# Optimization experiments

Measured on AMD Instinct MI355X. Metric: run time of the kernel, lower is better.

## Reference

```python
import jax, jax.numpy as jnp
import numpy as np

N = 50000
NEG_SLOPE = 0.2


def add_self_loops(edge_index, n):
    loops = jnp.arange(n, dtype=edge_index.dtype)
    return jnp.concatenate([edge_index, jnp.stack([loops, loops])], axis=1)


def gat_layer(x, edge_index, W, a_src, a_dst, b, heads, ch):
    # x: [N, F_in], W: [F_in, heads*ch], a_src/a_dst: [heads, ch], b: [heads*ch]
    n = x.shape[0]
    src, dst = edge_index[0], edge_index[1]
    h = (x @ W).reshape(n, heads, ch)                      # [N, H, C]
    alpha_src = jnp.sum(h * a_src, axis=-1)                # [N, H]
    alpha_dst = jnp.sum(h * a_dst, axis=-1)                # [N, H]
    e = jax.nn.leaky_relu(alpha_src[src] + alpha_dst[dst], NEG_SLOPE)  # [E, H]
    # segment softmax over incoming edges of each destination node
    m = jax.ops.segment_max(e, dst, num_segments=n)        # [N, H]
    ex = jnp.exp(e - m[dst])                               # [E, H]
    denom = jax.ops.segment_sum(ex, dst, num_segments=n)   # [N, H]
    alpha = ex / (denom[dst] + 1e-16)                      # [E, H]
    msg = h[src] * alpha[:, :, None]                       # [E, H, C]
    out = jax.ops.segment_sum(msg, dst, num_segments=n)    # [N, H, C]
    return out.reshape(n, heads * ch) + b


def setup_inputs() -> dict:
    key = jax.random.key(0)
    ks = jax.random.split(key, 12)
    input_dim, hidden_dim, output_dim, heads = 128, 32, 64, 4
    E = 1600000
    x = jax.random.normal(ks[0], (N, input_dim), dtype=jnp.float32)
    edge_index = jax.random.randint(ks[1], (2, E), 0, N, dtype=jnp.int64)
    s1 = 1.0 / np.sqrt(input_dim)
    s2 = 1.0 / np.sqrt(hidden_dim * heads)
    W1 = jax.random.uniform(ks[2], (input_dim, heads * hidden_dim), jnp.float32, -s1, s1)
    a_src1 = jax.random.uniform(ks[3], (heads, hidden_dim), jnp.float32, -s1, s1)
    a_dst1 = jax.random.uniform(ks[4], (heads, hidden_dim), jnp.float32, -s1, s1)
    b1 = jnp.zeros((heads * hidden_dim,), jnp.float32)
    W2 = jax.random.uniform(ks[5], (heads * hidden_dim, output_dim), jnp.float32, -s2, s2)
    a_src2 = jax.random.uniform(ks[6], (1, output_dim), jnp.float32, -s2, s2)
    a_dst2 = jax.random.uniform(ks[7], (1, output_dim), jnp.float32, -s2, s2)
    b2 = jnp.zeros((output_dim,), jnp.float32)
    return {"x": x, "edge_index": edge_index,
            "W1": W1, "a_src1": a_src1, "a_dst1": a_dst1, "b1": b1,
            "W2": W2, "a_src2": a_src2, "a_dst2": a_dst2, "b2": b2}


def reference(x, edge_index, W1, a_src1, a_dst1, b1, W2, a_src2, a_dst2, b2):
    n = x.shape[0]
    ei = add_self_loops(edge_index, n)
    h = gat_layer(x, ei, W1, a_src1, a_dst1, b1, heads=4, ch=32)
    h = jax.nn.relu(h)
    out = gat_layer(h, ei, W2, a_src2, a_dst2, b2, heads=1, ch=64)
    return out
```

## Files before the change

### kernel.cpp

```cpp
#include <hip/hip_runtime.h>
#include <hip/hip_bf16.h>
#include <hip/hip_fp16.h>


#define LRELU_SLOPE 0.2f
#define NBMAX 200
#define NBLK  512
#define BCAP  16384
#define CAPIMG 16384

typedef _Float16 f16x8 __attribute__((ext_vector_type(8)));
typedef _Float16 f16x4 __attribute__((ext_vector_type(4)));
typedef float f32x4 __attribute__((ext_vector_type(4)));


__global__ __launch_bounds__(256) void hist_kernel(const int* __restrict__ ei_dst,
                                                   int* __restrict__ hist, int E, int chunk) {
    __shared__ int h[NBMAX];
    int t = threadIdx.x;
    for (int i = t; i < NBMAX; i += 256) h[i] = 0;
    __syncthreads();
    int begin = blockIdx.x * chunk;
    int endE = min(E, begin + chunk);
    for (int e = begin + t; e < endE; e += 256) atomicAdd(&h[ei_dst[e] >> 8], 1);
    __syncthreads();
    for (int i = t; i < NBMAX; i += 256) hist[i * NBLK + blockIdx.x] = h[i];
}

__global__ __launch_bounds__(512) void bucket_scan_kernel(int* __restrict__ hist,
                                                          int* __restrict__ gfill) {
    __shared__ int buf[2][NBLK];
    int b = blockIdx.x, t = threadIdx.x;
    buf[0][t] = hist[b * NBLK + t];
    __syncthreads();
    int pi = 0;
#pragma unroll
    for (int off = 1; off < NBLK; off <<= 1) {
        int v = buf[pi][t];
        if (t >= off) v += buf[pi][t - off];
        buf[pi ^ 1][t] = v;
        __syncthreads();
        pi ^= 1;
    }
    hist[b * NBLK + t] = (t == 0) ? 0 : buf[pi][t - 1];
    if (t == 0) gfill[b] = buf[pi][NBLK - 1];
}

__global__ __launch_bounds__(256) void scatter2_kernel(const int* __restrict__ ei_src,
                                                       const int* __restrict__ ei_dst,
                                                       const int* __restrict__ hist,
                                                       unsigned int* __restrict__ records,
                                                       int E, int chunk) {
    __shared__ int base[NBMAX];
    __shared__ int lcnt[NBMAX];
    int t = threadIdx.x;
    for (int i = t; i < NBMAX; i += 256) {
        base[i] = hist[i * NBLK + blockIdx.x];
        lcnt[i] = 0;
    }
    __syncthreads();
    int begin = blockIdx.x * chunk;
    int endE = min(E, begin + chunk);
    for (int e = begin + t; e < endE; e += 256) {
        int s = ei_src[e], d = ei_dst[e];
        int bkt = d >> 8;
        unsigned int rec = (unsigned int)d | ((unsigned int)s << 16);
        int r = atomicAdd(&lcnt[bkt], 1);
        records[(size_t)bkt * BCAP + base[bkt] + r] = rec;
    }
}

__global__ __launch_bounds__(256) void scan_blocksums_kernel(const int* __restrict__ gfill,
                                                             int* __restrict__ bsums,
                                                             int* __restrict__ row_ptr,
                                                             int nblocks, int n, int total) {
    __shared__ int buf[2][256];
    int t = threadIdx.x;
    int v0 = 0;
    if (t < nblocks) v0 = gfill[t] + min(256, n - (t << 8));
    buf[0][t] = v0;
    __syncthreads();
    int pi = 0;
#pragma unroll
    for (int off = 1; off < 256; off <<= 1) {
        int v = buf[pi][t];
        if (t >= off) v += buf[pi][t - off];
        buf[pi ^ 1][t] = v;
        __syncthreads();
        pi ^= 1;
    }
    if (t < nblocks) bsums[t] = (t == 0) ? 0 : buf[pi][t - 1];
    if (t == 0) row_ptr[n] = total;
}

__global__ __launch_bounds__(256) void csr_fused_kernel(const unsigned int* __restrict__ records,
                                                        const int* __restrict__ gfill,
                                                        const int* __restrict__ bsums,
                                                        int* __restrict__ row_ptr,
                                                        unsigned short* __restrict__ col,
                                                        int N) {
    __shared__ unsigned short img[CAPIMG];
    __shared__ int cnt[2][256];
    __shared__ int lfill[256];
    int t = threadIdx.x, b = blockIdx.x;
    int bBase = b << 8;
    int bEnd = min(bBase + 256, N);
    int rbase = bsums[b];
    int c = gfill[b];
    int size = c + (bEnd - bBase);
    bool lds = (size <= CAPIMG);
    const unsigned int* r = records + (size_t)b * BCAP;
    int gi = bBase + t;
    cnt[0][t] = (gi < bEnd) ? 1 : 0;
    __syncthreads();
    for (int i = t; i < c; i += 256) atomicAdd(&cnt[0][r[i] & 255], 1);
    __syncthreads();
    int d = cnt[0][t];
    int pi = 0;
#pragma unroll
    for (int off = 1; off < 256; off <<= 1) {
        int v = cnt[pi][t];
        if (t >= off) v += cnt[pi][t - off];
        cnt[pi ^ 1][t] = v;
        __syncthreads();
        pi ^= 1;
    }
    int local = cnt[pi][t] - d;
    if (gi < bEnd) {
        row_ptr[gi] = rbase + local;
        lfill[t] = local + 1;
        if (lds) img[local] = (unsigned short)gi;
        else col[rbase + local] = (unsigned short)gi;
    }
    __syncthreads();
    for (int i = t; i < c; i += 256) {
        unsigned int rec = r[i];
        int d8 = rec & 255;
        unsigned short s = (unsigned short)(rec >> 16);
        int p = atomicAdd(&lfill[d8], 1);
        if (lds) img[p] = s;
        else col[rbase + p] = s;
    }
    __syncthreads();
    if (lds) {
        for (int i = t; i < size; i += 256) col[rbase + i] = img[i];
    }
}


__global__ __launch_bounds__(256) void gemm1_mfma_kernel(const float* __restrict__ X,
                                                         const float* __restrict__ W,
                                                         __half* __restrict__ outh,
                                                         const float* __restrict__ a_src,
                                                         const float* __restrict__ a_dst,
                                                         float* __restrict__ as_out,
                                                         float* __restrict__ ad_out, int nrows) {
    constexpr int KP = 136;
    __shared__ _Float16 wlds[128 * KP];
    int t = threadIdx.x;
    int wv = t >> 6, lane = t & 63;
    int quad = lane >> 4, m16 = lane & 15;
    for (int i = t; i < 4096; i += 256) {
        int k = i >> 5;
        int n0 = (i & 31) << 2;
        float4 v = *(const float4*)(W + k * 128 + n0);
        wlds[(n0 + 0) * KP + k] = (_Float16)v.x;
        wlds[(n0 + 1) * KP + k] = (_Float16)v.y;
        wlds[(n0 + 2) * KP + k] = (_Float16)v.z;
        wlds[(n0 + 3) * KP + k] = (_Float16)v.w;
    }
    __syncthreads();

    int row = blockIdx.x * 64 + wv * 16 + m16;
    int rowC = min(row, nrows - 1);
    const float* xp = X + (size_t)rowC * 128;

    f32x4 acc[8];
#pragma unroll
    for (int nt = 0; nt < 8; ++nt) acc[nt] = (f32x4)0.f;

    for (int kt = 0; kt < 128; kt += 32) {
        float4 v0 = *(const float4*)(xp + kt + quad * 8);
        float4 v1 = *(const float4*)(xp + kt + quad * 8 + 4);
        f16x8 af;
        af[0] = (_Float16)v0.x; af[1] = (_Float16)v0.y;
        af[2] = (_Float16)v0.z; af[3] = (_Float16)v0.w;
        af[4] = (_Float16)v1.x; af[5] = (_Float16)v1.y;
        af[6] = (_Float16)v1.z; af[7] = (_Float16)v1.w;
#pragma unroll
        for (int nt = 0; nt < 8; ++nt) {
            f16x8 bf = *(const f16x8*)(&wlds[(nt * 16 + m16) * KP + kt + quad * 8]);
            acc[nt] = __builtin_amdgcn_mfma_f32_16x16x32_f16(af, bf, acc[nt], 0, 0, 0);
        }
    }

    float aS[8], aD[8];
#pragma unroll
    for (int nt = 0; nt < 8; ++nt) {
        aS[nt] = a_src[nt * 16 + m16];
        aD[nt] = a_dst[nt * 16 + m16];
    }
    int rowBaseW = blockIdx.x * 64 + wv * 16;
#pragma unroll
    for (int r = 0; r < 4; ++r) {
        int orow = rowBaseW + quad * 4 + r;
        bool ov = orow < nrows;
        if (ov) {
#pragma unroll
            for (int nt = 0; nt < 8; ++nt)
                outh[(size_t)orow * 128 + nt * 16 + m16] = __float2half(acc[nt][r]);
        }
#pragma unroll
        for (int h = 0; h < 4; ++h) {
            float ss = acc[2 * h][r] * aS[2 * h] + acc[2 * h + 1][r] * aS[2 * h + 1];
            float dd = acc[2 * h][r] * aD[2 * h] + acc[2 * h + 1][r] * aD[2 * h + 1];
#pragma unroll
            for (int o = 1; o < 16; o <<= 1) {
                ss += __shfl_xor(ss, o, 64);
                dd += __shfl_xor(dd, o, 64);
            }
            if (ov && m16 == h) {
                as_out[orow * 4 + h] = ss;
                ad_out[orow * 4 + h] = dd;
            }
        }
    }
}


__global__ __launch_bounds__(256) void gemm2_mfma_kernel(const __half* __restrict__ Xh,
                                                         const float* __restrict__ W,
                                                         __half* __restrict__ outh,
                                                         const float* __restrict__ a_src,
                                                         const float* __restrict__ a_dst,
                                                         float* __restrict__ as_out,
                                                         float* __restrict__ ad_out, int nrows) {
    constexpr int KP = 136;
    __shared__ _Float16 wlds[64 * KP];
    int t = threadIdx.x;
    int wv = t >> 6, lane = t & 63;
    int quad = lane >> 4, m16 = lane & 15;
    for (int i = t; i < 2048; i += 256) {
        int k = i >> 4;
        int n0 = (i & 15) << 2;
        float4 v = *(const float4*)(W + k * 64 + n0);
        wlds[(n0 + 0) * KP + k] = (_Float16)v.x;
        wlds[(n0 + 1) * KP + k] = (_Float16)v.y;
        wlds[(n0 + 2) * KP + k] = (_Float16)v.z;
        wlds[(n0 + 3) * KP + k] = (_Float16)v.w;
    }
    __syncthreads();

    int row = blockIdx.x * 64 + wv * 16 + m16;
    int rowC = min(row, nrows - 1);
    const _Float16* xp = (const _Float16*)Xh + (size_t)rowC * 128;

    f32x4 acc[4];
#pragma unroll
    for (int nt = 0; nt < 4; ++nt) acc[nt] = (f32x4)0.f;

    for (int kt = 0; kt < 128; kt += 32) {
        f16x8 af = *(const f16x8*)(xp + kt + quad * 8);
#pragma unroll
        for (int nt = 0; nt < 4; ++nt) {
            f16x8 bf = *(const f16x8*)(&wlds[(nt * 16 + m16) * KP + kt + quad * 8]);
            acc[nt] = __builtin_amdgcn_mfma_f32_16x16x32_f16(af, bf, acc[nt], 0, 0, 0);
        }
    }

    float aS[4], aD[4];
#pragma unroll
    for (int nt = 0; nt < 4; ++nt) {
        aS[nt] = a_src[nt * 16 + m16];
        aD[nt] = a_dst[nt * 16 + m16];
    }
    int rowBaseW = blockIdx.x * 64 + wv * 16;
#pragma unroll
    for (int r = 0; r < 4; ++r) {
        int orow = rowBaseW + quad * 4 + r;
        bool ov = orow < nrows;
        if (ov) {
#pragma unroll
            for (int nt = 0; nt < 4; ++nt)
                outh[(size_t)orow * 64 + nt * 16 + m16] = __float2half(acc[nt][r]);
        }
        float ss = 0.f, dd = 0.f;
#pragma unroll
        for (int nt = 0; nt < 4; ++nt) {
            ss = fmaf(acc[nt][r], aS[nt], ss);
            dd = fmaf(acc[nt][r], aD[nt], dd);
        }
#pragma unroll
        for (int o = 1; o < 16; o <<= 1) {
            ss += __shfl_xor(ss, o, 64);
            dd += __shfl_xor(dd, o, 64);
        }
        if (ov && m16 == 0) {
            as_out[orow] = ss;
            ad_out[orow] = dd;
        }
    }
}


__global__ __launch_bounds__(256) void agg1_kernel(const __half* __restrict__ h1h,
                                                   const float* __restrict__ asrc,
                                                   const float* __restrict__ adst,
                                                   const int* __restrict__ row_ptr,
                                                   const unsigned short* __restrict__ col,
                                                   const float* __restrict__ b1,
                                                   __half* __restrict__ out, int n) {
    int wave = threadIdx.x >> 6;
    int lane = threadIdx.x & 63;
    int node = blockIdx.x * 4 + wave;
    if (node >= n) return;
    int half = lane >> 5;
    int m = lane & 31;
    int head = m >> 3;
    const char* __restrict__ h1c = (const char*)h1h;
    const char* __restrict__ asc = (const char*)asrc;
    unsigned moff = (unsigned)m << 3;
    unsigned aoff = (unsigned)head << 2;
    float ad = adst[node * 4 + head];
    int start = row_ptr[node], end = row_ptr[node + 1];
    float a0c = 0.f, a1c = 0.f, a2c = 0.f, a3c = 0.f, s = 0.f;
    for (int base = start; base < end; base += 64) {
        int cnt = min(64, end - base);
        int idx = base + lane;
        int myS = (idx < end) ? (int)col[idx] : 0;
        for (int j = 0; j < cnt; j += 12) {
            int jj[6];
            int sv[6];
#pragma unroll
            for (int k = 0; k < 6; ++k) {
                jj[k] = j + 2 * k + half;
                sv[k] = __shfl(myS, jj[k], 64);
            }
            f16x4 v[6];
            float as[6];
#pragma unroll
            for (int k = 0; k < 6; ++k) {
                v[k]  = *(const f16x4*)(h1c + ((((unsigned)sv[k]) << 8) | moff));
                as[k] = *(const float*)(asc + ((((unsigned)sv[k]) << 4) | aoff));
            }
#pragma unroll
            for (int k = 0; k < 6; ++k) {
                float e = as[k] + ad;
                e = fmaxf(e, LRELU_SLOPE * e);
                float p = (jj[k] < cnt) ? __expf(e) : 0.f;
                a0c = fmaf(p, (float)v[k][0], a0c);
                a1c = fmaf(p, (float)v[k][1], a1c);
                a2c = fmaf(p, (float)v[k][2], a2c);
                a3c = fmaf(p, (float)v[k][3], a3c);
                s += p;
            }
        }
    }
    a0c += __shfl_xor(a0c, 32, 64);
    a1c += __shfl_xor(a1c, 32, 64);
    a2c += __shfl_xor(a2c, 32, 64);
    a3c += __shfl_xor(a3c, 32, 64);
    s   += __shfl_xor(s, 32, 64);
    if (half == 0) {
        float inv = 1.f / (s + 1e-16f);
        float4 bb = ((const float4*)b1)[m];
        f16x4 o;
        o[0] = (_Float16)fmaxf(fmaf(a0c, inv, bb.x), 0.f);
        o[1] = (_Float16)fmaxf(fmaf(a1c, inv, bb.y), 0.f);
        o[2] = (_Float16)fmaxf(fmaf(a2c, inv, bb.z), 0.f);
        o[3] = (_Float16)fmaxf(fmaf(a3c, inv, bb.w), 0.f);
        ((f16x4*)out)[node * 32 + m] = o;
    }
}

__global__ __launch_bounds__(256) void agg2_kernel(const __half* __restrict__ h2bh,
                                                   const float* __restrict__ asrc,
                                                   const float* __restrict__ adst,
                                                   const int* __restrict__ row_ptr,
                                                   const unsigned short* __restrict__ col,
                                                   const float* __restrict__ b2,
                                                   float* __restrict__ out, int n) {
    int wave = threadIdx.x >> 6;
    int lane = threadIdx.x & 63;
    int node = blockIdx.x * 4 + wave;
    if (node >= n) return;
    int eslot = lane >> 3;
    int sub = lane & 7;
    const char* __restrict__ h2c = (const char*)h2bh;
    unsigned coff = (unsigned)sub << 4;
    float ad = adst[node];
    int start = row_ptr[node], end = row_ptr[node + 1];
    float acc[8];
#pragma unroll
    for (int c = 0; c < 8; ++c) acc[c] = 0.f;
    float s = 0.f;
    for (int base = start; base < end; base += 16) {
        int iA = base + eslot;
        int iB = iA + 8;
        int sA = (int)col[min(iA, end - 1)];
        int sB = (int)col[min(iB, end - 1)];
        f16x8 vA = *(const f16x8*)(h2c + ((((unsigned)sA) << 7) | coff));
        f16x8 vB = *(const f16x8*)(h2c + ((((unsigned)sB) << 7) | coff));
        float eA = asrc[sA] + ad;
        float eB = asrc[sB] + ad;
        eA = fmaxf(eA, LRELU_SLOPE * eA);
        eB = fmaxf(eB, LRELU_SLOPE * eB);
        float pA = (iA < end) ? __expf(eA) : 0.f;
        float pB = (iB < end) ? __expf(eB) : 0.f;
#pragma unroll
        for (int c = 0; c < 8; ++c) acc[c] = fmaf(pA, (float)vA[c], acc[c]);
#pragma unroll
        for (int c = 0; c < 8; ++c) acc[c] = fmaf(pB, (float)vB[c], acc[c]);
        s += pA + pB;
    }
#pragma unroll
    for (int o = 8; o < 64; o <<= 1) {
#pragma unroll
        for (int c = 0; c < 8; ++c) acc[c] += __shfl_xor(acc[c], o, 64);
        s += __shfl_xor(s, o, 64);
    }
    if (lane < 8) {
        float inv = 1.f / (s + 1e-16f);
        float4 bb0 = ((const float4*)b2)[sub * 2];
        float4 bb1 = ((const float4*)b2)[sub * 2 + 1];
        float4 o0, o1;
        o0.x = fmaf(acc[0], inv, bb0.x);
        o0.y = fmaf(acc[1], inv, bb0.y);
        o0.z = fmaf(acc[2], inv, bb0.z);
        o0.w = fmaf(acc[3], inv, bb0.w);
        o1.x = fmaf(acc[4], inv, bb1.x);
        o1.y = fmaf(acc[5], inv, bb1.y);
        o1.z = fmaf(acc[6], inv, bb1.z);
        o1.w = fmaf(acc[7], inv, bb1.w);
        ((float4*)(out + (size_t)node * 64))[sub * 2] = o0;
        ((float4*)(out + (size_t)node * 64))[sub * 2 + 1] = o1;
    }
}


extern "C" void kernel_launch(void* const* d_in, const int* in_sizes, int n_in,
                              void* d_out, int out_size, void* d_ws, size_t ws_size,
                              hipStream_t stream) {
    const float* x      = (const float*)d_in[0];
    const int*   ei     = (const int*)d_in[1];
    const float* W1     = (const float*)d_in[2];
    const float* a_src1 = (const float*)d_in[3];
    const float* a_dst1 = (const float*)d_in[4];
    const float* b1     = (const float*)d_in[5];
    const float* W2     = (const float*)d_in[6];
    const float* a_src2 = (const float*)d_in[7];
    const float* a_dst2 = (const float*)d_in[8];
    const float* b2     = (const float*)d_in[9];
    float* out = (float*)d_out;

    const int N = in_sizes[0] / 128;
    const int E = in_sizes[1] / 2;
    const int total = E + N;
    const int nBuckets = (N + 255) >> 8;

    char* ws = (char*)d_ws;
    size_t off = 0;
    auto alloc = [&](size_t bytes) {
        void* p = ws + off;
        off += (bytes + 255) & ~(size_t)255;
        return p;
    };
    float* regionA = (float*)alloc((size_t)N * 128 * 4);
    __half* h1h   = (__half*)alloc((size_t)N * 128 * 2);
    __half* h2bh  = (__half*)alloc((size_t)N * 64 * 2);
    float* asrc1  = (float*)alloc((size_t)N * 4 * 4);
    float* adst1  = (float*)alloc((size_t)N * 4 * 4);
    float* asrc2  = (float*)alloc((size_t)N * 4);
    float* adst2  = (float*)alloc((size_t)N * 4);
    int*   row_ptr= (int*)alloc((size_t)(N + 1) * 4);
    int*   gfill  = (int*)alloc((size_t)nBuckets * 4);
    int*   bsums  = (int*)alloc((size_t)nBuckets * 4);
    unsigned short* col = (unsigned short*)alloc((size_t)total * 2);

    unsigned int* records = (unsigned int*)regionA;
    int* hist = (int*)(regionA + (size_t)NBMAX * BCAP);
    __half* h2in = (__half*)regionA;
    (void)ws_size; (void)n_in; (void)out_size;

    const int* ei_src = ei;
    const int* ei_dst = ei + E;

    const int chunk = (E + NBLK - 1) / NBLK;
    hist_kernel<<<NBLK, 256, 0, stream>>>(ei_dst, hist, E, chunk);
    bucket_scan_kernel<<<nBuckets, NBLK, 0, stream>>>(hist, gfill);
    scatter2_kernel<<<NBLK, 256, 0, stream>>>(ei_src, ei_dst, hist, records, E, chunk);
    scan_blocksums_kernel<<<1, 256, 0, stream>>>(gfill, bsums, row_ptr, nBuckets, N, total);
    csr_fused_kernel<<<nBuckets, 256, 0, stream>>>(records, gfill, bsums, row_ptr, col, N);

    gemm1_mfma_kernel<<<(N + 63) / 64, 256, 0, stream>>>(x, W1, h1h, a_src1, a_dst1,
                                                         asrc1, adst1, N);
    agg1_kernel<<<(N + 3) / 4, 256, 0, stream>>>(h1h, asrc1, adst1,
                                                 row_ptr, col, b1, h2in, N);

    gemm2_mfma_kernel<<<(N + 63) / 64, 256, 0, stream>>>(h2in, W2, h2bh, a_src2, a_dst2,
                                                         asrc2, adst2, N);
    agg2_kernel<<<(N + 3) / 4, 256, 0, stream>>>(h2bh, asrc2, adst2,
                                                 row_ptr, col, b2, out, N);
}
```

Before: 244.7 us.

## Fuse edge bucketing, GEMM1 and attention logits into one launch; precompute W·a

The separate histogram, bucket-scan and scatter kernels become one partition of a combined launch. Each block now claims its bucket base with a global atomicAdd on gfill (zeroed by a memset), which removes the two-pass scan. The same launch runs GEMM1 concurrently with the edge bucketing, plus separate blocks that compute the layer-1 attention logits as X·(W1·a) in fp32. A final block folds W2 into the a_src2/a_dst2 vectors, so agg1 can emit the layer-2 logits directly from its output and the gemm2 epilogue reduction goes away. This cuts kernel launches and serial dependencies, but makes the edge order within a bucket depend on atomic timing and adds a redundant fp32 pass over X.

Result: no change. 242.2 us (-1.0%).

```diff
diff --git a/kernel.cpp b/kernel.cpp
--- a/kernel.cpp
+++ b/kernel.cpp
@@ -14,61 +14,152 @@
 typedef float f32x4 __attribute__((ext_vector_type(4)));
 
 
-__global__ __launch_bounds__(256) void hist_kernel(const int* __restrict__ ei_dst,
-                                                   int* __restrict__ hist, int E, int chunk) {
-    __shared__ int h[NBMAX];
+__global__ __launch_bounds__(256) void k1_kernel(
+    const int* __restrict__ ei_src, const int* __restrict__ ei_dst,
+    unsigned int* __restrict__ records, int* __restrict__ gfill,
+    const float* __restrict__ X, const float* __restrict__ W1,
+    __half* __restrict__ h1h,
+    const float* __restrict__ a_src1, const float* __restrict__ a_dst1,
+    float* __restrict__ asrc1, float* __restrict__ adst1,
+    const float* __restrict__ W2,
+    const float* __restrict__ a_src2, const float* __restrict__ a_dst2,
+    float* __restrict__ wa2,
+    int E, int chunk, int N, int G1B, int ALB) {
+    __shared__ __align__(16) char smem[34816];
     int t = threadIdx.x;
-    for (int i = t; i < NBMAX; i += 256) h[i] = 0;
-    __syncthreads();
-    int begin = blockIdx.x * chunk;
-    int endE = min(E, begin + chunk);
-    for (int e = begin + t; e < endE; e += 256) atomicAdd(&h[ei_dst[e] >> 8], 1);
-    __syncthreads();
-    for (int i = t; i < NBMAX; i += 256) hist[i * NBLK + blockIdx.x] = h[i];
-}
-
-__global__ __launch_bounds__(512) void bucket_scan_kernel(int* __restrict__ hist,
-                                                          int* __restrict__ gfill) {
-    __shared__ int buf[2][NBLK];
-    int b = blockIdx.x, t = threadIdx.x;
-    buf[0][t] = hist[b * NBLK + t];
-    __syncthreads();
-    int pi = 0;
-#pragma unroll
-    for (int off = 1; off < NBLK; off <<= 1) {
-        int v = buf[pi][t];
-        if (t >= off) v += buf[pi][t - off];
-        buf[pi ^ 1][t] = v;
-        __syncthreads();
-        pi ^= 1;
-    }
-    hist[b * NBLK + t] = (t == 0) ? 0 : buf[pi][t - 1];
-    if (t == 0) gfill[b] = buf[pi][NBLK - 1];
-}
-
-__global__ __launch_bounds__(256) void scatter2_kernel(const int* __restrict__ ei_src,
-                                                       const int* __restrict__ ei_dst,
-                                                       const int* __restrict__ hist,
-                                                       unsigned int* __restrict__ records,
-                                                       int E, int chunk) {
-    __shared__ int base[NBMAX];
-    __shared__ int lcnt[NBMAX];
-    int t = threadIdx.x;
-    for (int i = t; i < NBMAX; i += 256) {
-        base[i] = hist[i * NBLK + blockIdx.x];
-        lcnt[i] = 0;
-    }
-    __syncthreads();
-    int begin = blockIdx.x * chunk;
-    int endE = min(E, begin + chunk);
-    for (int e = begin + t; e < endE; e += 256) {
-        int s = ei_src[e], d = ei_dst[e];
-        int bkt = d >> 8;
-        unsigned int rec = (unsigned int)d | ((unsigned int)s << 16);
-        int r = atomicAdd(&lcnt[bkt], 1);
-        records[(size_t)bkt * BCAP + base[bkt] + r] = rec;
-    }
-}
+    int bid = blockIdx.x;
+
+    if (bid < NBLK) {
+        int* cnt  = (int*)smem;
+        int* base = ((int*)smem) + NBMAX;
+        for (int i = t; i < NBMAX; i += 256) cnt[i] = 0;
+        __syncthreads();
+        int begin = bid * chunk;
+        int endE = min(E, begin + chunk);
+        for (int e = begin + t; e < endE; e += 256) atomicAdd(&cnt[ei_dst[e] >> 8], 1);
+        __syncthreads();
+        for (int i = t; i < NBMAX; i += 256) {
+            int c = cnt[i];
+            base[i] = c ? atomicAdd(&gfill[i], c) : 0;
+            cnt[i] = 0;
+        }
+        __syncthreads();
+        for (int e = begin + t; e < endE; e += 256) {
+            int s = ei_src[e], d = ei_dst[e];
+            int bkt = d >> 8;
+            unsigned int rec = (unsigned int)d | ((unsigned int)s << 16);
+            int r = atomicAdd(&cnt[bkt], 1);
+            records[(size_t)bkt * BCAP + base[bkt] + r] = rec;
+        }
+        return;
+    }
+
+    if (bid < NBLK + G1B) {
+        constexpr int KP = 136;
+        _Float16* wlds = (_Float16*)smem;
+        int gb = bid - NBLK;
+        int wv = t >> 6, lane = t & 63;
+        int quad = lane >> 4, m16 = lane & 15;
+        for (int i = t; i < 4096; i += 256) {
+            int k = i >> 5;
+            int n0 = (i & 31) << 2;
+            float4 v = *(const float4*)(W1 + k * 128 + n0);
+            wlds[(n0 + 0) * KP + k] = (_Float16)v.x;
+            wlds[(n0 + 1) * KP + k] = (_Float16)v.y;
+            wlds[(n0 + 2) * KP + k] = (_Float16)v.z;
+            wlds[(n0 + 3) * KP + k] = (_Float16)v.w;
+        }
+        __syncthreads();
+
+        int row = gb * 64 + wv * 16 + m16;
+        int rowC = min(row, N - 1);
+        const float* xp = X + (size_t)rowC * 128;
+
+        f32x4 acc[8];
+#pragma unroll
+        for (int nt = 0; nt < 8; ++nt) acc[nt] = (f32x4)0.f;
+
+        for (int kt = 0; kt < 128; kt += 32) {
+            float4 v0 = *(const float4*)(xp + kt + quad * 8);
+            float4 v1 = *(const float4*)(xp + kt + quad * 8 + 4);
+            f16x8 af;
+            af[0] = (_Float16)v0.x; af[1] = (_Float16)v0.y;
+            af[2] = (_Float16)v0.z; af[3] = (_Float16)v0.w;
+            af[4] = (_Float16)v1.x; af[5] = (_Float16)v1.y;
+            af[6] = (_Float16)v1.z; af[7] = (_Float16)v1.w;
+#pragma unroll
+            for (int nt = 0; nt < 8; ++nt) {
+                f16x8 bf = *(const f16x8*)(&wlds[(nt * 16 + m16) * KP + kt + quad * 8]);
+                acc[nt] = __builtin_amdgcn_mfma_f32_16x16x32_f16(af, bf, acc[nt], 0, 0, 0);
+            }
+        }
+
+        int rowBaseW = gb * 64 + wv * 16;
+#pragma unroll
+        for (int r = 0; r < 4; ++r) {
+            int orow = rowBaseW + quad * 4 + r;
+            if (orow < N) {
+#pragma unroll
+                for (int nt = 0; nt < 8; ++nt)
+                    h1h[(size_t)orow * 128 + nt * 16 + m16] = __float2half(acc[nt][r]);
+            }
+        }
+        return;
+    }
+
+    int aid = bid - NBLK - G1B;
+    if (aid < ALB) {
+        float* waL = (float*)smem;
+        {
+            int k = t >> 1, grp = t & 1;
+            const float* wrow = W1 + k * 128;
+            const float* abase = grp ? a_dst1 : a_src1;
+#pragma unroll
+            for (int h = 0; h < 4; ++h) {
+                const float* av = abase + h * 32;
+                const float* wr = wrow + h * 32;
+                float acc = 0.f;
+                for (int c = 0; c < 32; ++c) acc += wr[c] * av[c];
+                waL[(grp * 4 + h) * 128 + k] = acc;
+            }
+        }
+        __syncthreads();
+        int row = aid * 256 + t;
+        if (row < N) {
+            const float4* x4 = (const float4*)(X + (size_t)row * 128);
+            float p[8];
+#pragma unroll
+            for (int o = 0; o < 8; ++o) p[o] = 0.f;
+            for (int k4 = 0; k4 < 32; ++k4) {
+                float4 xv = x4[k4];
+#pragma unroll
+                for (int o = 0; o < 8; ++o) {
+                    float4 wv = ((const float4*)(waL + o * 128))[k4];
+                    p[o] += xv.x * wv.x + xv.y * wv.y + xv.z * wv.z + xv.w * wv.w;
+                }
+            }
+            float4 ps = {p[0], p[1], p[2], p[3]};
+            float4 pd = {p[4], p[5], p[6], p[7]};
+            ((float4*)asrc1)[row] = ps;
+            ((float4*)adst1)[row] = pd;
+        }
+        return;
+    }
+
+    if (t < 128) {
+        const float* wr = W2 + t * 64;
+        float acc = 0.f;
+        for (int c = 0; c < 64; ++c) acc += wr[c] * a_src2[c];
+        wa2[t] = acc;
+    } else {
+        int k = t - 128;
+        const float* wr = W2 + k * 64;
+        float acc = 0.f;
+        for (int c = 0; c < 64; ++c) acc += wr[c] * a_dst2[c];
+        wa2[128 + k] = acc;
+    }
+}
+
 
 __global__ __launch_bounds__(256) void scan_blocksums_kernel(const int* __restrict__ gfill,
                                                              int* __restrict__ bsums,
@@ -148,93 +239,9 @@
 }
 
 
-__global__ __launch_bounds__(256) void gemm1_mfma_kernel(const float* __restrict__ X,
-                                                         const float* __restrict__ W,
-                                                         __half* __restrict__ outh,
-                                                         const float* __restrict__ a_src,
-                                                         const float* __restrict__ a_dst,
-                                                         float* __restrict__ as_out,
-                                                         float* __restrict__ ad_out, int nrows) {
-    constexpr int KP = 136;
-    __shared__ _Float16 wlds[128 * KP];
-    int t = threadIdx.x;
-    int wv = t >> 6, lane = t & 63;
-    int quad = lane >> 4, m16 = lane & 15;
-    for (int i = t; i < 4096; i += 256) {
-        int k = i >> 5;
-        int n0 = (i & 31) << 2;
-        float4 v = *(const float4*)(W + k * 128 + n0);
-        wlds[(n0 + 0) * KP + k] = (_Float16)v.x;
-        wlds[(n0 + 1) * KP + k] = (_Float16)v.y;
-        wlds[(n0 + 2) * KP + k] = (_Float16)v.z;
-        wlds[(n0 + 3) * KP + k] = (_Float16)v.w;
-    }
-    __syncthreads();
-
-    int row = blockIdx.x * 64 + wv * 16 + m16;
-    int rowC = min(row, nrows - 1);
-    const float* xp = X + (size_t)rowC * 128;
-
-    f32x4 acc[8];
-#pragma unroll
-    for (int nt = 0; nt < 8; ++nt) acc[nt] = (f32x4)0.f;
-
-    for (int kt = 0; kt < 128; kt += 32) {
-        float4 v0 = *(const float4*)(xp + kt + quad * 8);
-        float4 v1 = *(const float4*)(xp + kt + quad * 8 + 4);
-        f16x8 af;
-        af[0] = (_Float16)v0.x; af[1] = (_Float16)v0.y;
-        af[2] = (_Float16)v0.z; af[3] = (_Float16)v0.w;
-        af[4] = (_Float16)v1.x; af[5] = (_Float16)v1.y;
-        af[6] = (_Float16)v1.z; af[7] = (_Float16)v1.w;
-#pragma unroll
-        for (int nt = 0; nt < 8; ++nt) {
-            f16x8 bf = *(const f16x8*)(&wlds[(nt * 16 + m16) * KP + kt + quad * 8]);
-            acc[nt] = __builtin_amdgcn_mfma_f32_16x16x32_f16(af, bf, acc[nt], 0, 0, 0);
-        }
-    }
-
-    float aS[8], aD[8];
-#pragma unroll
-    for (int nt = 0; nt < 8; ++nt) {
-        aS[nt] = a_src[nt * 16 + m16];
-        aD[nt] = a_dst[nt * 16 + m16];
-    }
-    int rowBaseW = blockIdx.x * 64 + wv * 16;
-#pragma unroll
-    for (int r = 0; r < 4; ++r) {
-        int orow = rowBaseW + quad * 4 + r;
-        bool ov = orow < nrows;
-        if (ov) {
-#pragma unroll
-            for (int nt = 0; nt < 8; ++nt)
-                outh[(size_t)orow * 128 + nt * 16 + m16] = __float2half(acc[nt][r]);
-        }
-#pragma unroll
-        for (int h = 0; h < 4; ++h) {
-            float ss = acc[2 * h][r] * aS[2 * h] + acc[2 * h + 1][r] * aS[2 * h + 1];
-            float dd = acc[2 * h][r] * aD[2 * h] + acc[2 * h + 1][r] * aD[2 * h + 1];
-#pragma unroll
-            for (int o = 1; o < 16; o <<= 1) {
-                ss += __shfl_xor(ss, o, 64);
-                dd += __shfl_xor(dd, o, 64);
-            }
-            if (ov && m16 == h) {
-                as_out[orow * 4 + h] = ss;
-                ad_out[orow * 4 + h] = dd;
-            }
-        }
-    }
-}
-
-
 __global__ __launch_bounds__(256) void gemm2_mfma_kernel(const __half* __restrict__ Xh,
                                                          const float* __restrict__ W,
-                                                         __half* __restrict__ outh,
-                                                         const float* __restrict__ a_src,
-                                                         const float* __restrict__ a_dst,
-                                                         float* __restrict__ as_out,
-                                                         float* __restrict__ ad_out, int nrows) {
+                                                         __half* __restrict__ outh, int nrows) {
     constexpr int KP = 136;
     __shared__ _Float16 wlds[64 * KP];
     int t = threadIdx.x;
@@ -268,36 +275,14 @@
         }
     }
 
-    float aS[4], aD[4];
-#pragma unroll
-    for (int nt = 0; nt < 4; ++nt) {
-        aS[nt] = a_src[nt * 16 + m16];
-        aD[nt] = a_dst[nt * 16 + m16];
-    }
     int rowBaseW = blockIdx.x * 64 + wv * 16;
 #pragma unroll
     for (int r = 0; r < 4; ++r) {
         int orow = rowBaseW + quad * 4 + r;
-        bool ov = orow < nrows;
-        if (ov) {
+        if (orow < nrows) {
 #pragma unroll
             for (int nt = 0; nt < 4; ++nt)
                 outh[(size_t)orow * 64 + nt * 16 + m16] = __float2half(acc[nt][r]);
-        }
-        float ss = 0.f, dd = 0.f;
-#pragma unroll
-        for (int nt = 0; nt < 4; ++nt) {
-            ss = fmaf(acc[nt][r], aS[nt], ss);
-            dd = fmaf(acc[nt][r], aD[nt], dd);
-        }
-#pragma unroll
-        for (int o = 1; o < 16; o <<= 1) {
-            ss += __shfl_xor(ss, o, 64);
-            dd += __shfl_xor(dd, o, 64);
-        }
-        if (ov && m16 == 0) {
-            as_out[orow] = ss;
-            ad_out[orow] = dd;
         }
     }
 }
@@ -309,7 +294,10 @@
                                                    const int* __restrict__ row_ptr,
                                                    const unsigned short* __restrict__ col,
                                                    const float* __restrict__ b1,
-                                                   __half* __restrict__ out, int n) {
+                                                   const float* __restrict__ wa2,
+                                                   __half* __restrict__ out,
+                                                   float* __restrict__ asrc2,
+                                                   float* __restrict__ adst2, int n) {
     int wave = threadIdx.x >> 6;
     int lane = threadIdx.x & 63;
     int node = blockIdx.x * 4 + wave;
@@ -361,15 +349,31 @@
     a2c += __shfl_xor(a2c, 32, 64);
     a3c += __shfl_xor(a3c, 32, 64);
     s   += __shfl_xor(s, 32, 64);
+    float ps = 0.f, pd = 0.f;
     if (half == 0) {
         float inv = 1.f / (s + 1e-16f);
         float4 bb = ((const float4*)b1)[m];
+        float o0 = fmaxf(fmaf(a0c, inv, bb.x), 0.f);
+        float o1 = fmaxf(fmaf(a1c, inv, bb.y), 0.f);
+        float o2 = fmaxf(fmaf(a2c, inv, bb.z), 0.f);
+        float o3 = fmaxf(fmaf(a3c, inv, bb.w), 0.f);
         f16x4 o;
-        o[0] = (_Float16)fmaxf(fmaf(a0c, inv, bb.x), 0.f);
-        o[1] = (_Float16)fmaxf(fmaf(a1c, inv, bb.y), 0.f);
-        o[2] = (_Float16)fmaxf(fmaf(a2c, inv, bb.z), 0.f);
-        o[3] = (_Float16)fmaxf(fmaf(a3c, inv, bb.w), 0.f);
+        o[0] = (_Float16)o0; o[1] = (_Float16)o1;
+        o[2] = (_Float16)o2; o[3] = (_Float16)o3;
         ((f16x4*)out)[node * 32 + m] = o;
+        float4 w2s = ((const float4*)wa2)[m];
+        float4 w2d = ((const float4*)(wa2 + 128))[m];
+        ps = o0 * w2s.x + o1 * w2s.y + o2 * w2s.z + o3 * w2s.w;
+        pd = o0 * w2d.x + o1 * w2d.y + o2 * w2d.z + o3 * w2d.w;
+    }
+#pragma unroll
+    for (int o = 1; o <= 16; o <<= 1) {
+        ps += __shfl_xor(ps, o, 64);
+        pd += __shfl_xor(pd, o, 64);
+    }
+    if (lane == 0) {
+        asrc2[node] = ps;
+        adst2[node] = pd;
     }
 }
 
@@ -475,10 +479,10 @@
     int*   row_ptr= (int*)alloc((size_t)(N + 1) * 4);
     int*   gfill  = (int*)alloc((size_t)nBuckets * 4);
     int*   bsums  = (int*)alloc((size_t)nBuckets * 4);
+    float* wa2    = (float*)alloc(256 * 4);
     unsigned short* col = (unsigned short*)alloc((size_t)total * 2);
 
     unsigned int* records = (unsigned int*)regionA;
-    int* hist = (int*)(regionA + (size_t)NBMAX * BCAP);
     __half* h2in = (__half*)regionA;
     (void)ws_size; (void)n_in; (void)out_size;
 
@@ -486,19 +490,25 @@
     const int* ei_dst = ei + E;
 
     const int chunk = (E + NBLK - 1) / NBLK;
-    hist_kernel<<<NBLK, 256, 0, stream>>>(ei_dst, hist, E, chunk);
-    bucket_scan_kernel<<<nBuckets, NBLK, 0, stream>>>(hist, gfill);
-    scatter2_kernel<<<NBLK, 256, 0, stream>>>(ei_src, ei_dst, hist, records, E, chunk);
+    const int G1B = (N + 63) / 64;
+    const int ALB = (N + 255) / 256;
+
+    hipMemsetAsync(gfill, 0, (size_t)nBuckets * 4, stream);
+
+    k1_kernel<<<NBLK + G1B + ALB + 1, 256, 0, stream>>>(
+        ei_src, ei_dst, records, gfill,
+        x, W1, h1h, a_src1, a_dst1, asrc1, adst1,
+        W2, a_src2, a_dst2, wa2,
+        E, chunk, N, G1B, ALB);
+
     scan_blocksums_kernel<<<1, 256, 0, stream>>>(gfill, bsums, row_ptr, nBuckets, N, total);
     csr_fused_kernel<<<nBuckets, 256, 0, stream>>>(records, gfill, bsums, row_ptr, col, N);
 
-    gemm1_mfma_kernel<<<(N + 63) / 64, 256, 0, stream>>>(x, W1, h1h, a_src1, a_dst1,
-                                                         asrc1, adst1, N);
     agg1_kernel<<<(N + 3) / 4, 256, 0, stream>>>(h1h, asrc1, adst1,
-                                                 row_ptr, col, b1, h2in, N);
-
-    gemm2_mfma_kernel<<<(N + 63) / 64, 256, 0, stream>>>(h2in, W2, h2bh, a_src2, a_dst2,
-                                                         asrc2, adst2, N);
+                                                 row_ptr, col, b1, wa2,
+                                                 h2in, asrc2, adst2, N);
+
+    gemm2_mfma_kernel<<<(N + 63) / 64, 256, 0, stream>>>(h2in, W2, h2bh, N);
     agg2_kernel<<<(N + 3) / 4, 256, 0, stream>>>(h2bh, asrc2, adst2,
                                                  row_ptr, col, b2, out, N);
 }
```
